# Optimization experiments

Measured on AMD Instinct MI355X. Metric: run time of the kernel, lower is better.

## Reference

```python
import jax, jax.numpy as jnp
import numpy as np

B, S, D = 4, 2048, 1024
H = 16            # n_heads
HD = D // H       # head_dim = 64
F = 64            # feature_dim of linear-attention feature map


def setup_inputs() -> dict:
    key = jax.random.key(0)
    ks = jax.random.split(key, 16)
    w = lambda k, shape: jax.random.normal(k, shape, dtype=jnp.float32) * 0.02
    return {
        "x": jax.random.normal(ks[0], (B, S, D), dtype=jnp.float32),
        # flash-attention branch params (Linear stored as [in, out])
        "fq": w(ks[1], (D, D)),
        "fk": w(ks[2], (D, D)),
        "fv": w(ks[3], (D, D)),
        "fo_w": w(ks[4], (D, D)),
        "fo_b": jnp.zeros((D,), jnp.float32),
        # linear-attention branch params
        "lq": w(ks[5], (D, D)),
        "lk": w(ks[6], (D, D)),
        "lv": w(ks[7], (D, D)),
        "lo_w": w(ks[8], (D, D)),
        "lo_b": jnp.zeros((D,), jnp.float32),
        "fm_w": w(ks[9], (HD, F)),
        "fm_b": jnp.zeros((F,), jnp.float32),
        # gate
        "gate_w": w(ks[10], (D, 1)),
        "gate_b": jnp.zeros((1,), jnp.float32),
    }


def reference(x, fq, fk, fv, fo_w, fo_b, lq, lk, lv, lo_w, lo_b,
              fm_w, fm_b, gate_w, gate_b):
    b, s, d = x.shape
    # ---- flash (standard softmax) attention path ----
    q = (x @ fq).reshape(b, s, H, HD)
    k = (x @ fk).reshape(b, s, H, HD)
    v = (x @ fv).reshape(b, s, H, HD)
    scale = 1.0 / np.sqrt(HD).astype(np.float32)
    scores = jnp.einsum('bqhd,bkhd->bhqk', q, k) * scale
    attn = jax.nn.softmax(scores, axis=-1)
    flash = jnp.einsum('bhqk,bkhd->bqhd', attn, v).reshape(b, s, d)
    flash_out = flash @ fo_w + fo_b
    # ---- linear (kernelized) attention path ----
    ql = (x @ lq).reshape(b, s, H, HD)
    kl = (x @ lk).reshape(b, s, H, HD)
    vl = (x @ lv).reshape(b, s, H, HD)
    qf = jax.nn.relu(ql @ fm_w + fm_b)   # [b,s,h,f]
    kf = jax.nn.relu(kl @ fm_w + fm_b)
    kv = jnp.einsum('blhf,blhd->bhfd', kf, vl)
    lin = jnp.einsum('blhf,bhfd->blhd', qf, kv)
    k_sum = kf.sum(axis=1)                               # [b,h,f]
    norm = jnp.einsum('blhf,bhf->blh', qf, k_sum)[..., None]
    lin = lin / jnp.maximum(norm, 1e-6)
    linear_out = lin.reshape(b, s, d) @ lo_w + lo_b
    # ---- sigmoid gate blend ----
    gate = jax.nn.sigmoid(x @ gate_w + gate_b)           # [b,s,1]
    return gate * flash_out + (1.0 - gate) * linear_out
```

## Files before the change

kernel.cpp:

```cpp
#include <hip/hip_runtime.h>
#include <math.h>

typedef __attribute__((ext_vector_type(4))) float f32x4;
typedef __attribute__((ext_vector_type(16))) float f32x16;
typedef __attribute__((ext_vector_type(8))) short s16x8;
typedef __attribute__((ext_vector_type(8))) unsigned short u16x8;

constexpr int Bc = 4, Sc = 2048, Dc = 1024, Hc = 16, HDc = 64, Fc = 64;
constexpr int Rc = Bc * Sc;
constexpr size_t MAT = (size_t)Rc * Dc;
constexpr int KST = 88;
constexpr int NCH = 16;

__device__ __forceinline__ float bf2f(unsigned short u) {
    union { unsigned int i; float f; } v; v.i = ((unsigned int)u) << 16; return v.f;
}
__device__ __forceinline__ unsigned short f2bf(float f) {
    union { float f; unsigned int i; } v; v.f = f;
    unsigned int r = v.i + 0x7FFFu + ((v.i >> 16) & 1u);
    return (unsigned short)(r >> 16);
}
__device__ __forceinline__ unsigned cvtpk(float a, float b) {
    unsigned r;
    asm("v_cvt_pk_bf16_f32 %0, %1, %2" : "=v"(r) : "v"(a), "v"(b));
    return r;
}
__device__ __forceinline__ void async16(const void* g, void* l) {
    __builtin_amdgcn_global_load_lds(
        (const __attribute__((address_space(1))) unsigned int*)g,
        (__attribute__((address_space(3))) unsigned int*)l, 16, 0, 0);
}

__global__ __launch_bounds__(256) void gate_cvt(const float* __restrict__ x,
        const float* __restrict__ gw, const float* __restrict__ gb,
        float* __restrict__ G, unsigned short* __restrict__ Y) {
    const int lane = threadIdx.x & 63;
    const int wave = threadIdx.x >> 6;
    const int r = blockIdx.x * 4 + wave;
    const size_t base = (size_t)r * Dc;
    float acc = 0.f;
    #pragma unroll
    for (int i = 0; i < 4; ++i) {
        int off = (lane + 64 * i) * 4;
        float4 v = *(const float4*)(x + base + off);
        float4 w = *(const float4*)(gw + off);
        acc += v.x * w.x + v.y * w.y + v.z * w.z + v.w * w.w;
        ushort4 o;
        o.x = f2bf(v.x); o.y = f2bf(v.y); o.z = f2bf(v.z); o.w = f2bf(v.w);
        *(ushort4*)(Y + base + off) = o;
    }
    #pragma unroll
    for (int off = 32; off > 0; off >>= 1) acc += __shfl_down(acc, off, 64);
    if (lane == 0) {
        float z = acc + gb[0];
        G[r] = 1.f / (1.f + __expf(-z));
    }
}

__global__ __launch_bounds__(256) void wtrans(
        const float* W0, const float* W1, const float* W2, const float* W3,
        const float* W4, const float* W5, const float* W6, const float* W7,
        unsigned short* T0, unsigned short* T1, unsigned short* T2, unsigned short* T3,
        unsigned short* T4, unsigned short* T5, unsigned short* T6, unsigned short* T7) {
    const float* W; unsigned short* T;
    switch (blockIdx.z) {
        case 0: W = W0; T = T0; break;  case 1: W = W1; T = T1; break;
        case 2: W = W2; T = T2; break;  case 3: W = W3; T = T3; break;
        case 4: W = W4; T = T4; break;  case 5: W = W5; T = T5; break;
        case 6: W = W6; T = T6; break;  default: W = W7; T = T7; break;
    }
    __shared__ float tile[64][65];
    const int t = threadIdx.x;
    const int r0 = blockIdx.x * 64, c0 = blockIdx.y * 64;
    #pragma unroll
    for (int i = 0; i < 4; ++i) {
        int row = (t >> 4) + 16 * i, col = (t & 15) * 4;
        float4 v = *(const float4*)(W + (size_t)(r0 + row) * 1024 + c0 + col);
        tile[row][col] = v.x; tile[row][col + 1] = v.y;
        tile[row][col + 2] = v.z; tile[row][col + 3] = v.w;
    }
    __syncthreads();
    #pragma unroll
    for (int i = 0; i < 4; ++i) {
        int orow = (t >> 4) + 16 * i, ocol = (t & 15) * 4;
        ushort4 o;
        o.x = f2bf(tile[ocol][orow]);     o.y = f2bf(tile[ocol + 1][orow]);
        o.z = f2bf(tile[ocol + 2][orow]); o.w = f2bf(tile[ocol + 3][orow]);
        *(ushort4*)(T + (size_t)(c0 + orow) * 1024 + r0 + ocol) = o;
    }
}

__global__ __launch_bounds__(256) void gemm3(const unsigned short* __restrict__ A,
        const unsigned short* __restrict__ WT, unsigned short* __restrict__ C0,
        unsigned short* __restrict__ C1, unsigned short* __restrict__ C2) {
    __shared__ unsigned short As[128 * 32];
    __shared__ unsigned short Bs[128 * 32];
    const int tid = threadIdx.x, wave = tid >> 6, lane = tid & 63;
    const int brow = blockIdx.x * 128;
    const int bcolg = blockIdx.y * 128;
    unsigned short* C = (blockIdx.y < 8) ? C0 : (blockIdx.y < 16 ? C1 : C2);
    const int bcol = bcolg & 1023;
    const int wm = wave >> 1, wn = wave & 1;
    const int lr = lane & 15, g8 = (lane >> 4) * 8;
    const int srow = 32 * wave + (lane >> 2);
    const int scol = (lane & 3) * 8;
    f32x4 acc[4][4];
    #pragma unroll
    for (int m = 0; m < 4; ++m)
        #pragma unroll
        for (int n = 0; n < 4; ++n) acc[m][n] = (f32x4){0.f, 0.f, 0.f, 0.f};
    for (int k0 = 0; k0 < 1024; k0 += 32) {
        __syncthreads();
        #pragma unroll
        for (int i = 0; i < 2; ++i) {
            async16(A  + (size_t)(brow  + srow + 16 * i) * 1024 + k0 + scol, &As[(32 * wave + 16 * i) * 32]);
            async16(WT + (size_t)(bcolg + srow + 16 * i) * 1024 + k0 + scol, &Bs[(32 * wave + 16 * i) * 32]);
        }
        __syncthreads();
        s16x8 af[4], bf[4];
        #pragma unroll
        for (int m = 0; m < 4; ++m) af[m] = *(const s16x8*)&As[(64 * wm + 16 * m + lr) * 32 + g8];
        #pragma unroll
        for (int n = 0; n < 4; ++n) bf[n] = *(const s16x8*)&Bs[(64 * wn + 16 * n + lr) * 32 + g8];
        #pragma unroll
        for (int m = 0; m < 4; ++m)
            #pragma unroll
            for (int n = 0; n < 4; ++n)
                acc[m][n] = __builtin_amdgcn_mfma_f32_16x16x32_bf16(af[m], bf[n], acc[m][n], 0, 0, 0);
    }
    const int rg = (lane >> 4) * 4;
    #pragma unroll
    for (int m = 0; m < 4; ++m)
        #pragma unroll
        for (int n = 0; n < 4; ++n)
            #pragma unroll
            for (int j = 0; j < 4; ++j)
                C[(size_t)(brow + 64 * wm + 16 * m + rg + j) * 1024 + bcol + 64 * wn + 16 * n + lr] =
                    f2bf(acc[m][n][j]);
}

__global__ __launch_bounds__(256) void final_gemm(const unsigned short* __restrict__ A1,
        const unsigned short* __restrict__ WT1, const unsigned short* __restrict__ A2,
        const unsigned short* __restrict__ WT2, const float* __restrict__ b1,
        const float* __restrict__ b2, const float* __restrict__ G, float* __restrict__ OUT) {
    __shared__ unsigned short As[128 * 32];
    __shared__ unsigned short Bs[128 * 32];
    const int tid = threadIdx.x, wave = tid >> 6, lane = tid & 63;
    const int brow = blockIdx.x * 128, bcol = blockIdx.y * 128;
    const int wm = wave >> 1, wn = wave & 1;
    const int lr = lane & 15, g8 = (lane >> 4) * 8;
    const int srow = 32 * wave + (lane >> 2);
    const int scol = (lane & 3) * 8;
    f32x4 acc[4][4];
    #pragma unroll
    for (int m = 0; m < 4; ++m)
        #pragma unroll
        for (int n = 0; n < 4; ++n) acc[m][n] = (f32x4){0.f, 0.f, 0.f, 0.f};
    for (int pass = 0; pass < 2; ++pass) {
        const unsigned short* A  = pass ? A2 : A1;
        const unsigned short* WT = pass ? WT2 : WT1;
        for (int k0 = 0; k0 < 1024; k0 += 32) {
            __syncthreads();
            #pragma unroll
            for (int i = 0; i < 2; ++i) {
                async16(A  + (size_t)(brow + srow + 16 * i) * 1024 + k0 + scol, &As[(32 * wave + 16 * i) * 32]);
                async16(WT + (size_t)(bcol + srow + 16 * i) * 1024 + k0 + scol, &Bs[(32 * wave + 16 * i) * 32]);
            }
            __syncthreads();
            s16x8 af[4], bf[4];
            #pragma unroll
            for (int m = 0; m < 4; ++m) af[m] = *(const s16x8*)&As[(64 * wm + 16 * m + lr) * 32 + g8];
            #pragma unroll
            for (int n = 0; n < 4; ++n) bf[n] = *(const s16x8*)&Bs[(64 * wn + 16 * n + lr) * 32 + g8];
            #pragma unroll
            for (int m = 0; m < 4; ++m)
                #pragma unroll
                for (int n = 0; n < 4; ++n)
                    acc[m][n] = __builtin_amdgcn_mfma_f32_16x16x32_bf16(af[m], bf[n], acc[m][n], 0, 0, 0);
        }
    }
    const int rg = (lane >> 4) * 4;
    #pragma unroll
    for (int m = 0; m < 4; ++m)
        #pragma unroll
        for (int j = 0; j < 4; ++j) {
            int row = brow + 64 * wm + 16 * m + rg + j;
            float g = G[row];
            #pragma unroll
            for (int n = 0; n < 4; ++n) {
                int col = bcol + 64 * wn + 16 * n + lr;
                OUT[(size_t)row * 1024 + col] = acc[m][n][j] + g * b1[col] + (1.f - g) * b2[col];
            }
        }
}

__global__ __launch_bounds__(512) void flash_mfma(const unsigned short* __restrict__ Qg,
        const unsigned short* __restrict__ Kg, const unsigned short* __restrict__ Vg,
        const float* __restrict__ G, unsigned short* __restrict__ FA) {
    __shared__ unsigned short Ks[2][64 * KST];
    __shared__ unsigned short Vt[2][64 * KST];
    const int tid = threadIdx.x, wave = tid >> 6, lane = tid & 63;
    const int b = blockIdx.z, h = blockIdx.y, q0 = blockIdx.x * 256;
    const int lq = lane & 31, hi = lane >> 5;
    const float QSCALE = 0.125f * 1.44269504f;
    const size_t qrow = (size_t)b * Sc + q0 + wave * 32 + lq;
    const size_t qoff = qrow * Dc + h * HDc + 8 * hi;
    s16x8 aq[4];
    #pragma unroll
    for (int dc = 0; dc < 4; ++dc) {
        u16x8 raw = *(const u16x8*)(Qg + qoff + 16 * dc);
        #pragma unroll
        for (int j = 0; j < 8; ++j) aq[dc][j] = (short)f2bf(bf2f(raw[j]) * QSCALE);
    }
    const s16x8 ones = {0x3F80, 0x3F80, 0x3F80, 0x3F80, 0x3F80, 0x3F80, 0x3F80, 0x3F80};
    f32x16 oacc[2], lacc;
    #pragma unroll
    for (int t = 0; t < 2; ++t)
        #pragma unroll
        for (int r = 0; r < 16; ++r) oacc[t][r] = 0.f;
    #pragma unroll
    for (int r = 0; r < 16; ++r) lacc[r] = 0.f;
    const int srow = tid >> 3, sc8 = (tid & 7) * 8, va = tid & 7;
    const int p0 = (srow & 3) | (((srow >> 3) & 1) << 2) | (((srow >> 2) & 1) << 3) | (srow & 0x30);
    const int pg = p0 >> 3, pin = p0 & 7;
    const size_t kvoff = (size_t)h * HDc + sc8;
    {
        size_t gg = ((size_t)b * Sc + srow) * Dc + kvoff;
        u16x8 kreg = *(const u16x8*)(Kg + gg);
        u16x8 vreg = *(const u16x8*)(Vg + gg);
        *(u16x8*)&Ks[0][srow * KST + sc8] = kreg;
        #pragma unroll
        for (int j = 0; j < 8; ++j)
            Vt[0][(sc8 + j) * KST + 8 * (pg ^ va) + pin] = vreg[j];
    }
    __syncthreads();
    int cur = 0;
    for (int t0 = 0; t0 < Sc; t0 += 64) {
        const bool nxt = (t0 + 64) < Sc;
        u16x8 kn, vn;
        if (nxt) {
            size_t gg = ((size_t)b * Sc + t0 + 64 + srow) * Dc + kvoff;
            kn = *(const u16x8*)(Kg + gg);
            vn = *(const u16x8*)(Vg + gg);
        }
        f32x16 s2[2];
        #pragma unroll
        for (int t = 0; t < 2; ++t)
            #pragma unroll
            for (int r = 0; r < 16; ++r) s2[t][r] = 0.f;
        __builtin_amdgcn_s_setprio(1);
        #pragma unroll
        for (int kt2 = 0; kt2 < 2; ++kt2)
            #pragma unroll
            for (int dc = 0; dc < 4; ++dc) {
                s16x8 ak = *(const s16x8*)&Ks[cur][(32 * kt2 + lq) * KST + 16 * dc + 8 * hi];
                s2[kt2] = __builtin_amdgcn_mfma_f32_32x32x16_bf16(ak, aq[dc], s2[kt2], 0, 0, 0);
            }
        __builtin_amdgcn_s_setprio(0);
        #pragma unroll
        for (int t = 0; t < 2; ++t)
            #pragma unroll
            for (int r = 0; r < 16; ++r)
                s2[t][r] = exp2f(s2[t][r]);
        s16x8 pf[4];
        #pragma unroll
        for (int kc = 0; kc < 4; ++kc) {
            const int t = kc >> 1, e = 8 * (kc & 1);
            union { s16x8 v; unsigned u[4]; } w;
            w.u[0] = cvtpk(s2[t][e + 0], s2[t][e + 1]);
            w.u[1] = cvtpk(s2[t][e + 2], s2[t][e + 3]);
            w.u[2] = cvtpk(s2[t][e + 4], s2[t][e + 5]);
            w.u[3] = cvtpk(s2[t][e + 6], s2[t][e + 7]);
            pf[kc] = w.v;
        }
        __builtin_amdgcn_s_setprio(1);
        #pragma unroll
        for (int dtile = 0; dtile < 2; ++dtile) {
            const int row = 32 * dtile + lq;
            const int rsw = (row >> 3) & 7;
            #pragma unroll
            for (int kc = 0; kc < 4; ++kc) {
                const int g = 4 * (kc >> 1) + 2 * (kc & 1) + hi;
                s16x8 av = *(const s16x8*)&Vt[cur][row * KST + 8 * (g ^ rsw)];
                oacc[dtile] = __builtin_amdgcn_mfma_f32_32x32x16_bf16(av, pf[kc], oacc[dtile], 0, 0, 0);
            }
        }
        #pragma unroll
        for (int kc = 0; kc < 4; ++kc)
            lacc = __builtin_amdgcn_mfma_f32_32x32x16_bf16(ones, pf[kc], lacc, 0, 0, 0);
        __builtin_amdgcn_s_setprio(0);
        if (nxt) {
            *(u16x8*)&Ks[cur ^ 1][srow * KST + sc8] = kn;
            #pragma unroll
            for (int j = 0; j < 8; ++j)
                Vt[cur ^ 1][(sc8 + j) * KST + 8 * (pg ^ va) + pin] = vn[j];
        }
        __syncthreads();
        cur ^= 1;
    }
    const float scl = G[qrow] / lacc[0];
    #pragma unroll
    for (int dtile = 0; dtile < 2; ++dtile)
        #pragma unroll
        for (int s = 0; s < 4; ++s) {
            ushort4 o4;
            o4.x = f2bf(oacc[dtile][4 * s + 0] * scl);
            o4.y = f2bf(oacc[dtile][4 * s + 1] * scl);
            o4.z = f2bf(oacc[dtile][4 * s + 2] * scl);
            o4.w = f2bf(oacc[dtile][4 * s + 3] * scl);
            *(ushort4*)(FA + qrow * Dc + h * HDc + 32 * dtile + 8 * s + 4 * hi) = o4;
        }
}

__global__ __launch_bounds__(256) void featmap_kernel(unsigned short* __restrict__ QL,
        unsigned short* __restrict__ KL, const float* __restrict__ fmw, const float* __restrict__ fmb) {
    __shared__ float Wf[64][68];
    __shared__ float bs[64];
    __shared__ float Xs[16][68];
    const int tid = threadIdx.x;
    for (int i = tid; i < 64 * 64 / 4; i += 256) {
        int r = i >> 4, c = (i & 15) << 2;
        *(float4*)&Wf[r][c] = *(const float4*)(fmw + r * 64 + c);
    }
    if (tid < 64) bs[tid] = fmb[tid];
    const size_t row0 = (size_t)blockIdx.x * 16;
    const int rr = tid >> 4;
    const int fg = (tid & 15) << 2;
    for (int pass = 0; pass < 2; ++pass) {
        unsigned short* X = pass ? KL : QL;
        __syncthreads();
        {
            int r = tid >> 4, c = (tid & 15) << 2;
            ushort4 xv = *(const ushort4*)(X + (row0 + r) * 64 + c);
            Xs[r][c] = bf2f(xv.x); Xs[r][c + 1] = bf2f(xv.y);
            Xs[r][c + 2] = bf2f(xv.z); Xs[r][c + 3] = bf2f(xv.w);
        }
        __syncthreads();
        float a0 = bs[fg], a1 = bs[fg + 1], a2 = bs[fg + 2], a3 = bs[fg + 3];
        #pragma unroll 8
        for (int d = 0; d < 64; ++d) {
            float xv = Xs[rr][d];
            float4 w = *(const float4*)&Wf[d][fg];
            a0 += xv * w.x; a1 += xv * w.y; a2 += xv * w.z; a3 += xv * w.w;
        }
        ushort4 ov;
        ov.x = f2bf(fmaxf(a0, 0.f)); ov.y = f2bf(fmaxf(a1, 0.f));
        ov.z = f2bf(fmaxf(a2, 0.f)); ov.w = f2bf(fmaxf(a3, 0.f));
        *(ushort4*)(X + (row0 + rr) * 64 + fg) = ov;
    }
}

__global__ __launch_bounds__(256) void kv_part(const unsigned short* __restrict__ KF,
        const unsigned short* __restrict__ VL, float* __restrict__ PART, float* __restrict__ PARTS) {
    __shared__ float Ks[32][68];
    __shared__ float Vs[32][68];
    const int tid = threadIdx.x;
    const int bh = blockIdx.x;
    const int b = bh >> 4, h = bh & 15;
    const int ch = blockIdx.y;
    const int f = tid >> 2;
    const int dg = (tid & 3) << 4;
    float acc[16] = {};
    float ksum = 0.f;
    const int lbeg = ch * (Sc / NCH), lend = lbeg + Sc / NCH;
    for (int l0 = lbeg; l0 < lend; l0 += 32) {
        __syncthreads();
        for (int i = tid; i < 32 * 64 / 4; i += 256) {
            int r = i >> 4, c = (i & 15) << 2;
            size_t gg = ((size_t)(b * Sc + l0 + r) * Hc + h) * 64 + c;
            ushort4 kk = *(const ushort4*)(KF + gg);
            ushort4 vv = *(const ushort4*)(VL + gg);
            Ks[r][c] = bf2f(kk.x); Ks[r][c + 1] = bf2f(kk.y);
            Ks[r][c + 2] = bf2f(kk.z); Ks[r][c + 3] = bf2f(kk.w);
            Vs[r][c] = bf2f(vv.x); Vs[r][c + 1] = bf2f(vv.y);
            Vs[r][c + 2] = bf2f(vv.z); Vs[r][c + 3] = bf2f(vv.w);
        }
        __syncthreads();
        #pragma unroll 4
        for (int ll = 0; ll < 32; ++ll) {
            float kf = Ks[ll][f];
            ksum += kf;
            float4 v0 = *(const float4*)&Vs[ll][dg];
            float4 v1 = *(const float4*)&Vs[ll][dg + 4];
            float4 v2 = *(const float4*)&Vs[ll][dg + 8];
            float4 v3 = *(const float4*)&Vs[ll][dg + 12];
            acc[0] += kf * v0.x; acc[1] += kf * v0.y; acc[2]  += kf * v0.z; acc[3]  += kf * v0.w;
            acc[4] += kf * v1.x; acc[5] += kf * v1.y; acc[6]  += kf * v1.z; acc[7]  += kf * v1.w;
            acc[8] += kf * v2.x; acc[9] += kf * v2.y; acc[10] += kf * v2.z; acc[11] += kf * v2.w;
            acc[12] += kf * v3.x; acc[13] += kf * v3.y; acc[14] += kf * v3.z; acc[15] += kf * v3.w;
        }
    }
    size_t o = (((size_t)ch * 64 + bh) * 64 + f) * 64 + dg;
    *(float4*)(PART + o)      = make_float4(acc[0], acc[1], acc[2], acc[3]);
    *(float4*)(PART + o + 4)  = make_float4(acc[4], acc[5], acc[6], acc[7]);
    *(float4*)(PART + o + 8)  = make_float4(acc[8], acc[9], acc[10], acc[11]);
    *(float4*)(PART + o + 12) = make_float4(acc[12], acc[13], acc[14], acc[15]);
    if ((tid & 3) == 0) PARTS[((size_t)ch * 64 + bh) * 64 + f] = ksum;
}

__global__ __launch_bounds__(256) void kv_reduce(const float* __restrict__ PART,
        float* __restrict__ KV) {
    size_t i = (size_t)blockIdx.x * 256 + threadIdx.x;
    float s = 0.f;
    #pragma unroll
    for (int ch = 0; ch < NCH; ++ch) s += PART[(size_t)ch * 262144 + i];
    KV[i] = s;
}
__global__ __launch_bounds__(256) void ks_reduce(const float* __restrict__ PARTS,
        float* __restrict__ KS) {
    int i = blockIdx.x * 256 + threadIdx.x;
    float s = 0.f;
    #pragma unroll
    for (int ch = 0; ch < NCH; ++ch) s += PARTS[ch * 4096 + i];
    KS[i] = s;
}

__global__ __launch_bounds__(256) void lin_kernel(const unsigned short* __restrict__ QF,
        const float* __restrict__ KV, const float* __restrict__ KSUM,
        const float* __restrict__ G, unsigned short* __restrict__ LA) {
    __shared__ float Qs[4][68];
    __shared__ float Ss[4][68];
    const int tid = threadIdx.x;
    const size_t i0 = (size_t)blockIdx.x * 4;
    {
        int r = tid >> 6, c = tid & 63;
        size_t i = i0 + r;
        int bh = (int)(i / ((size_t)Sc * Hc)) * Hc + (int)(i & (Hc - 1));
        Qs[r][c] = bf2f(QF[i * 64 + c]);
        Ss[r][c] = KSUM[(size_t)bh * 64 + c];
    }
    __syncthreads();
    const int r = tid >> 6, d = tid & 63;
    const size_t i = i0 + r;
    const int bh = (int)(i / ((size_t)Sc * Hc)) * Hc + (int)(i & (Hc - 1));
    const float* kvp = KV + (size_t)bh * 64 * 64 + d;
    float acc = 0.f, nrm = 0.f;
    #pragma unroll 8
    for (int ff = 0; ff < 64; ++ff) {
        float q = Qs[r][ff];
        acc += q * kvp[(size_t)ff * 64];
        nrm += q * Ss[r][ff];
    }
    float g = G[(int)(i >> 4)];
    LA[i * 64 + d] = f2bf((1.f - g) * acc / fmaxf(nrm, 1e-6f));
}

extern "C" void kernel_launch(void* const* d_in, const int* in_sizes, int n_in,
                              void* d_out, int out_size, void* d_ws, size_t ws_size,
                              hipStream_t stream) {
    const float* x   = (const float*)d_in[0];
    const float* fq  = (const float*)d_in[1];
    const float* fk  = (const float*)d_in[2];
    const float* fv  = (const float*)d_in[3];
    const float* fow = (const float*)d_in[4];
    const float* fob = (const float*)d_in[5];
    const float* lq  = (const float*)d_in[6];
    const float* lk  = (const float*)d_in[7];
    const float* lv  = (const float*)d_in[8];
    const float* low = (const float*)d_in[9];
    const float* lob = (const float*)d_in[10];
    const float* fmw = (const float*)d_in[11];
    const float* fmb = (const float*)d_in[12];
    const float* gw  = (const float*)d_in[13];
    const float* gb  = (const float*)d_in[14];
    float* out = (float*)d_out;

    char* p = (char*)d_ws;
    unsigned short* xb = (unsigned short*)p;          p += MAT * 2;
    unsigned short* wt_fq = (unsigned short*)p;       p += (size_t)1024 * 1024 * 2;
    unsigned short* wt_fk = (unsigned short*)p;       p += (size_t)1024 * 1024 * 2;
    unsigned short* wt_fv = (unsigned short*)p;       p += (size_t)1024 * 1024 * 2;
    unsigned short* wt_fo = (unsigned short*)p;       p += (size_t)1024 * 1024 * 2;
    unsigned short* wt_lq = (unsigned short*)p;       p += (size_t)1024 * 1024 * 2;
    unsigned short* wt_lk = (unsigned short*)p;       p += (size_t)1024 * 1024 * 2;
    unsigned short* wt_lv = (unsigned short*)p;       p += (size_t)1024 * 1024 * 2;
    unsigned short* wt_lo = (unsigned short*)p;       p += (size_t)1024 * 1024 * 2;
    unsigned short* P0 = (unsigned short*)p;          p += MAT * 2;
    unsigned short* P1 = (unsigned short*)p;          p += MAT * 2;
    unsigned short* P2 = (unsigned short*)p;          p += MAT * 2;
    unsigned short* FA = (unsigned short*)p;          p += MAT * 2;
    unsigned short* LA = (unsigned short*)p;          p += MAT * 2;
    float* KV = (float*)p;                            p += (size_t)Bc * Hc * Fc * HDc * 4;
    float* KS = (float*)p;                            p += (size_t)Bc * Hc * Fc * 4;
    float* G  = (float*)p;                            p += (size_t)Rc * 4;
    float* PART  = (float*)p;                         p += (size_t)NCH * 64 * 64 * 64 * 4;
    float* PARTS = (float*)p;                         p += (size_t)NCH * 64 * 64 * 4;

    dim3 proj3Grid(Rc / 128, 24);
    dim3 gemmGrid(Rc / 128, Dc / 128);

    gate_cvt<<<Rc / 4, 256, 0, stream>>>(x, gw, gb, G, xb);
    wtrans<<<dim3(16, 16, 8), 256, 0, stream>>>(fq, fk, fv, fow, lq, lk, lv, low,
            wt_fq, wt_fk, wt_fv, wt_fo, wt_lq, wt_lk, wt_lv, wt_lo);

    gemm3<<<proj3Grid, 256, 0, stream>>>(xb, wt_lq, P0, P1, P2);
    featmap_kernel<<<Rc * Hc / 16, 256, 0, stream>>>(P0, P1, fmw, fmb);
    kv_part<<<dim3(Bc * Hc, NCH), 256, 0, stream>>>(P1, P2, PART, PARTS);
    kv_reduce<<<(64 * 64 * 64) / 256, 256, 0, stream>>>(PART, KV);
    ks_reduce<<<(64 * 64) / 256, 256, 0, stream>>>(PARTS, KS);
    lin_kernel<<<Rc * Hc / 4, 256, 0, stream>>>(P0, KV, KS, G, LA);

    gemm3<<<proj3Grid, 256, 0, stream>>>(xb, wt_fq, P0, P1, P2);
    flash_mfma<<<dim3(Sc / 256, Hc, Bc), 512, 0, stream>>>(P0, P1, P2, G, FA);

    final_gemm<<<gemmGrid, 256, 0, stream>>>(FA, wt_fo, LA, wt_lo, fob, lob, G, out);
}
```

Measured before the change: 455.8 us.

## Replace scalar linear-attention apply with bf16 MFMA GEMM and remap flash grid

The per-row scalar lin_kernel, which reread fp32 KV from global memory for every output element, is replaced by a new prep kernel and an MFMA kernel. The prep kernel packs KV transposed plus k_sum as an extra column into a bf16 80x64 matrix per (batch, head). The MFMA kernel then computes the numerator and the normalizer together as one small GEMM over 128-row tiles and applies the gate scaling in its epilogue. Separately, the flash_mfma grid is reordered so batch and head vary fastest, which changes block scheduling order and likely cache reuse. KV and k_sum are now rounded to bf16, which reduces precision, and an extra small kernel launch is added.

```diff
diff --git a/kernel.cpp b/kernel.cpp
--- a/kernel.cpp
+++ b/kernel.cpp
@@ -200,7 +200,7 @@
     __shared__ unsigned short Ks[2][64 * KST];
     __shared__ unsigned short Vt[2][64 * KST];
     const int tid = threadIdx.x, wave = tid >> 6, lane = tid & 63;
-    const int b = blockIdx.z, h = blockIdx.y, q0 = blockIdx.x * 256;
+    const int b = blockIdx.x >> 4, h = blockIdx.x & 15, q0 = blockIdx.y * 256;
     const int lq = lane & 31, hi = lane >> 5;
     const float QSCALE = 0.125f * 1.44269504f;
     const size_t qrow = (size_t)b * Sc + q0 + wave * 32 + lq;
@@ -415,34 +415,73 @@
     KS[i] = s;
 }
 
-__global__ __launch_bounds__(256) void lin_kernel(const unsigned short* __restrict__ QF,
-        const float* __restrict__ KV, const float* __restrict__ KSUM,
-        const float* __restrict__ G, unsigned short* __restrict__ LA) {
-    __shared__ float Qs[4][68];
-    __shared__ float Ss[4][68];
-    const int tid = threadIdx.x;
-    const size_t i0 = (size_t)blockIdx.x * 4;
-    {
-        int r = tid >> 6, c = tid & 63;
-        size_t i = i0 + r;
-        int bh = (int)(i / ((size_t)Sc * Hc)) * Hc + (int)(i & (Hc - 1));
-        Qs[r][c] = bf2f(QF[i * 64 + c]);
-        Ss[r][c] = KSUM[(size_t)bh * 64 + c];
+__global__ __launch_bounds__(256) void kvb_build(const float* __restrict__ KV,
+        const float* __restrict__ KS, unsigned short* __restrict__ KVB) {
+    const int bh = blockIdx.x, t = threadIdx.x;
+    for (int i = t; i < 80 * 64; i += 256) {
+        int n = i >> 6, f = i & 63;
+        float v = (n < 64) ? KV[(size_t)bh * 4096 + f * 64 + n]
+                           : (n == 64 ? KS[bh * 64 + f] : 0.f);
+        KVB[(size_t)bh * 5120 + i] = f2bf(v);
+    }
+}
+
+__global__ __launch_bounds__(256) void lin_mfma(const unsigned short* __restrict__ QF,
+        const unsigned short* __restrict__ KVB, const float* __restrict__ G,
+        unsigned short* __restrict__ LA) {
+    __shared__ unsigned short As[128 * 72];
+    __shared__ unsigned short Bs[80 * 72];
+    const int tid = threadIdx.x, wave = tid >> 6, lane = tid & 63;
+    const int bh = blockIdx.y, b = bh >> 4, h = bh & 15;
+    const size_t rowg0 = (size_t)b * Sc + blockIdx.x * 128;
+    #pragma unroll
+    for (int i = 0; i < 4; ++i) {
+        int idx = tid + 256 * i;
+        int r = idx >> 3, c8 = (idx & 7) * 8;
+        *(u16x8*)&As[r * 72 + c8] = *(const u16x8*)(QF + (rowg0 + r) * 1024 + h * 64 + c8);
+    }
+    #pragma unroll
+    for (int i = 0; i < 3; ++i) {
+        int idx = tid + 256 * i;
+        if (idx < 640) {
+            int r = idx >> 3, c8 = (idx & 7) * 8;
+            *(u16x8*)&Bs[r * 72 + c8] = *(const u16x8*)(KVB + (size_t)bh * 5120 + r * 64 + c8);
+        }
     }
     __syncthreads();
-    const int r = tid >> 6, d = tid & 63;
-    const size_t i = i0 + r;
-    const int bh = (int)(i / ((size_t)Sc * Hc)) * Hc + (int)(i & (Hc - 1));
-    const float* kvp = KV + (size_t)bh * 64 * 64 + d;
-    float acc = 0.f, nrm = 0.f;
-    #pragma unroll 8
-    for (int ff = 0; ff < 64; ++ff) {
-        float q = Qs[r][ff];
-        acc += q * kvp[(size_t)ff * 64];
-        nrm += q * Ss[r][ff];
-    }
-    float g = G[(int)(i >> 4)];
-    LA[i * 64 + d] = f2bf((1.f - g) * acc / fmaxf(nrm, 1e-6f));
+    const int lr = lane & 15, g8 = (lane >> 4) * 8;
+    f32x4 acc[2][5];
+    #pragma unroll
+    for (int m = 0; m < 2; ++m)
+        #pragma unroll
+        for (int n = 0; n < 5; ++n) acc[m][n] = (f32x4){0.f, 0.f, 0.f, 0.f};
+    #pragma unroll
+    for (int kc = 0; kc < 2; ++kc) {
+        s16x8 af[2];
+        #pragma unroll
+        for (int m = 0; m < 2; ++m)
+            af[m] = *(const s16x8*)&As[(32 * wave + 16 * m + lr) * 72 + kc * 32 + g8];
+        #pragma unroll
+        for (int n = 0; n < 5; ++n) {
+            s16x8 bfv = *(const s16x8*)&Bs[(16 * n + lr) * 72 + kc * 32 + g8];
+            #pragma unroll
+            for (int m = 0; m < 2; ++m)
+                acc[m][n] = __builtin_amdgcn_mfma_f32_16x16x32_bf16(af[m], bfv, acc[m][n], 0, 0, 0);
+        }
+    }
+    const int rg = (lane >> 4) * 4;
+    #pragma unroll
+    for (int m = 0; m < 2; ++m)
+        #pragma unroll
+        for (int j = 0; j < 4; ++j) {
+            size_t rglob = rowg0 + 32 * wave + 16 * m + rg + j;
+            float g = G[rglob];
+            float nv = __shfl(acc[m][4][j], lane & 48, 64);
+            float inv = (1.f - g) / fmaxf(nv, 1e-6f);
+            #pragma unroll
+            for (int n = 0; n < 4; ++n)
+                LA[rglob * 1024 + h * 64 + 16 * n + lr] = f2bf(acc[m][n][j] * inv);
+        }
 }
 
 extern "C" void kernel_launch(void* const* d_in, const int* in_sizes, int n_in,
@@ -485,6 +524,7 @@
     float* G  = (float*)p;                            p += (size_t)Rc * 4;
     float* PART  = (float*)p;                         p += (size_t)NCH * 64 * 64 * 64 * 4;
     float* PARTS = (float*)p;                         p += (size_t)NCH * 64 * 64 * 4;
+    unsigned short* KVB = (unsigned short*)p;         p += (size_t)64 * 80 * 64 * 2;
 
     dim3 proj3Grid(Rc / 128, 24);
     dim3 gemmGrid(Rc / 128, Dc / 128);
@@ -498,10 +538,11 @@
     kv_part<<<dim3(Bc * Hc, NCH), 256, 0, stream>>>(P1, P2, PART, PARTS);
     kv_reduce<<<(64 * 64 * 64) / 256, 256, 0, stream>>>(PART, KV);
     ks_reduce<<<(64 * 64) / 256, 256, 0, stream>>>(PARTS, KS);
-    lin_kernel<<<Rc * Hc / 4, 256, 0, stream>>>(P0, KV, KS, G, LA);
+    kvb_build<<<64, 256, 0, stream>>>(KV, KS, KVB);
+    lin_mfma<<<dim3(Sc / 128, 64), 256, 0, stream>>>(P0, KVB, G, LA);
 
     gemm3<<<proj3Grid, 256, 0, stream>>>(xb, wt_fq, P0, P1, P2);
-    flash_mfma<<<dim3(Sc / 256, Hc, Bc), 512, 0, stream>>>(P0, P1, P2, G, FA);
+    flash_mfma<<<dim3(64, 8), 512, 0, stream>>>(P0, P1, P2, G, FA);
 
     final_gemm<<<gemmGrid, 256, 0, stream>>>(FA, wt_fo, LA, wt_lo, fob, lob, G, out);
 }
```

Result: faster. 386.1 us (-15.3%).
